# Performance work log

Measured on AMD Instinct MI355X. Metric: run time of the kernel, lower is better.

The kernel has to match this reference:

```python
import jax, jax.numpy as jnp
import numpy as np

B, T, DIM = 2, 2048, 2048
N_HEADS, N_KV_HEADS = 16, 4
HEAD_DIM = DIM // N_HEADS  # 128
N_REP = N_HEADS // N_KV_HEADS  # 4
ROPE_THETA = 10000.0


def setup_inputs() -> dict:
    key = jax.random.key(0)
    ks = jax.random.split(key, 5)
    x = jax.random.normal(ks[0], (B, T, DIM), dtype=jnp.float32)
    # RoPE tables (equivalent to complex freqs_cis = exp(i * t * inv_freq))
    inv_freq = 1.0 / (ROPE_THETA ** (np.arange(0, HEAD_DIM, 2, dtype=np.float32) / HEAD_DIM))
    t = np.arange(T, dtype=np.float32)
    ang = np.outer(t, inv_freq)  # (T, HEAD_DIM//2)
    freqs_cos = jnp.asarray(np.cos(ang), dtype=jnp.float32)
    freqs_sin = jnp.asarray(np.sin(ang), dtype=jnp.float32)
    s = 0.02
    wq = jax.random.normal(ks[1], (DIM, N_HEADS * HEAD_DIM), dtype=jnp.float32) * s
    wk = jax.random.normal(ks[2], (DIM, N_KV_HEADS * HEAD_DIM), dtype=jnp.float32) * s
    wv = jax.random.normal(ks[3], (DIM, N_KV_HEADS * HEAD_DIM), dtype=jnp.float32) * s
    wo = jax.random.normal(ks[4], (N_HEADS * HEAD_DIM, DIM), dtype=jnp.float32) * s
    return {"x": x, "freqs_cos": freqs_cos, "freqs_sin": freqs_sin,
            "wq": wq, "wk": wk, "wv": wv, "wo": wo}


def _apply_rope(t, cos, sin):
    # t: (B, H, T, hd); cos/sin: (T, hd//2); interleaved pairs like view_as_complex
    tr = t[..., 0::2]
    ti = t[..., 1::2]
    c = cos[None, None, :, :]
    s = sin[None, None, :, :]
    out_r = tr * c - ti * s
    out_i = tr * s + ti * c
    return jnp.stack([out_r, out_i], axis=-1).reshape(t.shape)


def reference(x, freqs_cos, freqs_sin, wq, wk, wv, wo):
    Bb, Tt, C = x.shape
    q = (x @ wq).reshape(Bb, Tt, N_HEADS, HEAD_DIM).transpose(0, 2, 1, 3)      # (B,H,T,hd)
    k = (x @ wk).reshape(Bb, Tt, N_KV_HEADS, HEAD_DIM).transpose(0, 2, 1, 3)   # (B,KV,T,hd)
    v = (x @ wv).reshape(Bb, Tt, N_KV_HEADS, HEAD_DIM).transpose(0, 2, 1, 3)
    q = _apply_rope(q, freqs_cos[:Tt], freqs_sin[:Tt])
    k = _apply_rope(k, freqs_cos[:Tt], freqs_sin[:Tt])
    # GQA repeat_kv
    k = jnp.repeat(k, N_REP, axis=1)  # (B,H,T,hd)
    v = jnp.repeat(v, N_REP, axis=1)
    scale = 1.0 / jnp.sqrt(jnp.float32(HEAD_DIM))
    scores = jnp.einsum("bhqd,bhkd->bhqk", q, k) * scale
    causal = jnp.tril(jnp.ones((Tt, Tt), dtype=bool))
    scores = jnp.where(causal[None, None], scores, jnp.float32(-jnp.inf))
    attn = jax.nn.softmax(scores, axis=-1)
    out = jnp.einsum("bhqk,bhkd->bhqd", attn, v)          # (B,H,T,hd)
    out = out.transpose(0, 2, 1, 3).reshape(Bb, Tt, C)
    return out @ wo
```

## Files before the change

kernel.cpp:

```cpp
#include <hip/hip_runtime.h>
#include <hip/hip_bf16.h>

#define SEQT 2048
#define NH 16
#define HD 128

typedef __bf16 bf16;
typedef __bf16 bf16x4 __attribute__((ext_vector_type(4)));
typedef __bf16 bf16x8 __attribute__((ext_vector_type(8)));
typedef float f32x4 __attribute__((ext_vector_type(4)));
typedef float f32x16 __attribute__((ext_vector_type(16)));

__device__ inline void glds16(const bf16* g, bf16* l) {
  __builtin_amdgcn_global_load_lds(
      (const __attribute__((address_space(1))) unsigned int*)g,
      (__attribute__((address_space(3))) unsigned int*)l, 16, 0, 0);
}

__device__ inline unsigned int cvtpk(float a, float b) {
  unsigned int d;
  asm("v_cvt_pk_bf16_f32 %0, %1, %2" : "=v"(d) : "v"(a), "v"(b));
  return d;
}

__global__ __launch_bounds__(256) void k_convert(const float* __restrict__ in,
                                                 bf16* __restrict__ out, int n8) {
  int i = blockIdx.x * 256 + threadIdx.x;
  if (i >= n8) return;
  const float4* p = (const float4*)in + (size_t)i * 2;
  float4 a = p[0], b = p[1];
  bf16x8 o;
  o[0] = (bf16)a.x; o[1] = (bf16)a.y; o[2] = (bf16)a.z; o[3] = (bf16)a.w;
  o[4] = (bf16)b.x; o[5] = (bf16)b.y; o[6] = (bf16)b.z; o[7] = (bf16)b.w;
  *((bf16x8*)out + i) = o;
}

__global__ __launch_bounds__(256) void k_transpose(const float* __restrict__ in,
                                                   bf16* __restrict__ out, int R, int C) {
  __shared__ float tile[32][33];
  int c0 = blockIdx.x * 32, r0 = blockIdx.y * 32;
  int tx = threadIdx.x, ty = threadIdx.y;
#pragma unroll
  for (int i = 0; i < 4; i++)
    tile[ty + i * 8][tx] = in[(size_t)(r0 + ty + i * 8) * C + c0 + tx];
  __syncthreads();
#pragma unroll
  for (int i = 0; i < 4; i++) {
    int r = ty + i * 8;
    out[(size_t)(c0 + r) * R + r0 + tx] = (bf16)tile[tx][r];
  }
}

__global__ __launch_bounds__(256) void k_transpose3(const float* __restrict__ wq,
                                                    const float* __restrict__ wk,
                                                    const float* __restrict__ wv,
                                                    bf16* __restrict__ W) {
  __shared__ float tile[32][33];
  int bx = blockIdx.x;
  const float* src;
  bf16* dst;
  int C;
  if (bx < 64) {
    src = wq; dst = W; C = 2048;
  } else if (bx < 80) {
    src = wk; dst = W + 2048 * 2048; C = 512; bx -= 64;
  } else {
    src = wv; dst = W + 2560 * 2048; C = 512; bx -= 80;
  }
  int c0 = bx * 32, r0 = blockIdx.y * 32;
  int tx = threadIdx.x, ty = threadIdx.y;
#pragma unroll
  for (int i = 0; i < 4; i++)
    tile[ty + i * 8][tx] = src[(size_t)(r0 + ty + i * 8) * C + c0 + tx];
  __syncthreads();
#pragma unroll
  for (int i = 0; i < 4; i++) {
    int r = ty + i * 8;
    dst[(size_t)(c0 + r) * 2048 + r0 + tx] = (bf16)tile[tx][r];
  }
}

template <typename OutT>
__global__ __launch_bounds__(256) void k_gemm(const bf16* __restrict__ A,
                                              const bf16* __restrict__ Bt,
                                              OutT* __restrict__ C,
                                              int M, int N, int K, int ldc) {
  __shared__ bf16 Al[128 * 32];
  __shared__ bf16 Bl[128 * 32];
  int tid = threadIdx.x;
  int m0 = blockIdx.y * 128, n0 = blockIdx.x * 128;
  int wid = tid >> 6, lane = tid & 63;
  int wr = (wid >> 1) * 64, wc = (wid & 1) * 64;
  int lr = lane & 15, lk = (lane >> 4) * 8;
  f32x4 acc[4][4] = {};

  for (int k0 = 0; k0 < K; k0 += 32) {
#pragma unroll
    for (int i = 0; i < 2; i++) {
      int idx = i * 256 + tid;
      int r = idx >> 2, kc = (idx & 3) * 8;
      glds16(A + (size_t)(m0 + r) * K + k0 + kc, Al + idx * 8);
      glds16(Bt + (size_t)(n0 + r) * K + k0 + kc, Bl + idx * 8);
    }
    __syncthreads();
    bf16x8 af[4], bfr[4];
#pragma unroll
    for (int mi = 0; mi < 4; mi++) af[mi] = *(const bf16x8*)&Al[(wr + mi * 16 + lr) * 32 + lk];
#pragma unroll
    for (int ni = 0; ni < 4; ni++) bfr[ni] = *(const bf16x8*)&Bl[(wc + ni * 16 + lr) * 32 + lk];
#pragma unroll
    for (int mi = 0; mi < 4; mi++)
#pragma unroll
      for (int ni = 0; ni < 4; ni++)
        acc[mi][ni] = __builtin_amdgcn_mfma_f32_16x16x32_bf16(af[mi], bfr[ni], acc[mi][ni], 0, 0, 0);
    __syncthreads();
  }

  int rbase = m0 + wr + ((lane >> 4) << 2);
#pragma unroll
  for (int mi = 0; mi < 4; mi++)
#pragma unroll
    for (int ni = 0; ni < 4; ni++)
#pragma unroll
      for (int r = 0; r < 4; r++) {
        int row = rbase + mi * 16 + r;
        int col = n0 + wc + ni * 16 + lr;
        C[(size_t)row * ldc + col] = (OutT)acc[mi][ni][r];
      }
}

__global__ __launch_bounds__(256) void k_rope(bf16* __restrict__ qkv,
                                              const float* __restrict__ fcos,
                                              const float* __restrict__ fsin) {
  int gid = blockIdx.x * 256 + threadIdx.x;
  int row = gid / 1280;
  int p = gid % 1280;
  int head = p >> 6;
  int dp = p & 63;
  int t = row & (SEQT - 1);
  int colbase = head < NH ? head * HD : NH * HD + (head - NH) * HD;
  bf16* ptr = qkv + (size_t)row * 3072 + colbase + dp * 2;
  float a = (float)ptr[0], b = (float)ptr[1];
  float c = fcos[t * 64 + dp], s = fsin[t * 64 + dp];
  ptr[0] = (bf16)(a * c - b * s);
  ptr[1] = (bf16)(a * s + b * c);
}

__global__ __launch_bounds__(256, 2) void k_attn(const bf16* __restrict__ qkv,
                                                 bf16* __restrict__ attout) {
  __shared__ bf16 Kl[2][8192];
  __shared__ bf16 Vt[128][72];
  __shared__ float Tabs[4][4][32];
  int bid = blockIdx.x;
  int qt = 31 - (bid >> 5);
  int bh = bid & 31;
  int b = bh >> 4, h = bh & 15, kvh = h >> 2;
  int tid = threadIdx.x, wid = tid >> 6, lane = tid & 63;
  int kvhalf = wid >> 1, wq = wid & 1;
  int li = lane & 31, hi = lane >> 5;
  int q0 = qt * 64;
  int qmin = q0 + wq * 32, qmax = qmin + 31;
  int qlane = qmin + li;
  const float C1 = 0.12751744979927212f;

  const bf16* kgbase = qkv + (size_t)b * SEQT * 3072 + 2048 + kvh * HD;
  const bf16* vgbase = kgbase + 512;

  bf16x8 qf[8];
  {
    const bf16* qb = qkv + (size_t)(b * SEQT + qlane) * 3072 + h * HD + hi * 8;
#pragma unroll
    for (int ks = 0; ks < 8; ks++) qf[ks] = *(const bf16x8*)(qb + ks * 16);
  }

  float mrun = -INFINITY, lpart = 0.f;
  f32x16 o0 = {}, o1 = {}, o2 = {}, o3 = {};
  int nkt = qt + 1;
  int kvbase = 32 * kvhalf;

  int g = (lane >> 4) & 3;
  int lr = lane & 15;
  int kq4 = (wid * 4 + g) * 4;
  int dc = lr * 8;
  int xr = (lr & 7) << 3;
  int kvw = kq4 ^ xr;

  bf16x8 vr0, vr1, vr2, vr3;

#pragma unroll
  for (int r = 0; r < 4; r++) {
    int ci = r * 256 + tid;
    int row = ci >> 4;
    int sl = (ci & 15) ^ (row & 15);
    glds16(kgbase + (size_t)row * 3072 + sl * 8, &Kl[0][ci * 8]);
  }
  {
    const bf16* vrow = vgbase + (size_t)kq4 * 3072 + dc;
    vr0 = *(const bf16x8*)(vrow);
    vr1 = *(const bf16x8*)(vrow + 3072);
    vr2 = *(const bf16x8*)(vrow + 6144);
    vr3 = *(const bf16x8*)(vrow + 9216);
  }

  for (int kt = 0; kt < nkt; kt++) {
    int cur = kt & 1;
    int kv0 = kt * 64;
    asm volatile("s_waitcnt vmcnt(0)" ::: "memory");

#pragma unroll
    for (int j = 0; j < 8; j++) {
      bf16x4 w;
      w[0] = vr0[j]; w[1] = vr1[j]; w[2] = vr2[j]; w[3] = vr3[j];
      *(bf16x4*)&Vt[dc + j][kvw] = w;
    }

    if (kt + 1 < nkt) {
      int kv1 = kv0 + 64;
      bf16* kdst = &Kl[cur ^ 1][0];
#pragma unroll
      for (int r = 0; r < 4; r++) {
        int ci = r * 256 + tid;
        int row = ci >> 4;
        int sl = (ci & 15) ^ (row & 15);
        glds16(kgbase + (size_t)(kv1 + row) * 3072 + sl * 8, kdst + ci * 8);
      }
      const bf16* vrow = vgbase + (size_t)(kv1 + kq4) * 3072 + dc;
      vr0 = *(const bf16x8*)(vrow);
      vr1 = *(const bf16x8*)(vrow + 3072);
      vr2 = *(const bf16x8*)(vrow + 6144);
      vr3 = *(const bf16x8*)(vrow + 9216);
    }

    asm volatile("s_waitcnt lgkmcnt(0)" ::: "memory");
    __builtin_amdgcn_sched_barrier(0);
    __builtin_amdgcn_s_barrier();
    __builtin_amdgcn_sched_barrier(0);

    if (kv0 + kvbase <= qmax) {
      f32x16 s0 = {};
      const char* kb0 = (const char*)&Kl[cur][0] + kvhalf * 8192 + li * 256;
      __builtin_amdgcn_s_setprio(1);
#pragma unroll
      for (int ks = 0; ks < 8; ks++) {
        int off = ((ks * 2 + hi) ^ (li & 15)) << 4;
        bf16x8 kf0 = *(const bf16x8*)(kb0 + off);
        s0 = __builtin_amdgcn_mfma_f32_32x32x16_bf16(kf0, qf[ks], s0, 0, 0, 0);
      }
      __builtin_amdgcn_s_setprio(0);

      if (kv0 + kvbase + 31 > qmin) {
        int base0 = kv0 + kvbase + 4 * hi - qlane;
#pragma unroll
        for (int r = 0; r < 16; r++) {
          int off = (r & 3) + 8 * (r >> 2);
          if (base0 + off > 0) s0[r] = -INFINITY;
        }
      }

      float pm = s0[0];
#pragma unroll
      for (int r = 1; r < 16; r++) pm = fmaxf(pm, s0[r]);
      pm = fmaxf(pm, __shfl_xor(pm, 32));

      if (!__all(pm - mrun <= 62.0f)) {
        float mnew = fmaxf(mrun, pm);
        float alpha = exp2f((mrun - mnew) * C1);
        mrun = mnew;
        lpart *= alpha;
        Tabs[0][wid][li] = alpha;
        asm volatile("s_waitcnt lgkmcnt(0)" ::: "memory");
        f32x4 a0 = *(const f32x4*)&Tabs[0][wid][4 * hi];
        f32x4 a1 = *(const f32x4*)&Tabs[0][wid][4 * hi + 8];
        f32x4 a2 = *(const f32x4*)&Tabs[0][wid][4 * hi + 16];
        f32x4 a3 = *(const f32x4*)&Tabs[0][wid][4 * hi + 24];
#define RESC_RR(rr, av)                                            \
  _Pragma("unroll") for (int i = 0; i < 4; i++) {                  \
    float f = av[i];                                               \
    o0[rr * 4 + i] *= f; o1[rr * 4 + i] *= f;                      \
    o2[rr * 4 + i] *= f; o3[rr * 4 + i] *= f;                      \
  }
        RESC_RR(0, a0) RESC_RR(1, a1) RESC_RR(2, a2) RESC_RR(3, a3)
#undef RESC_RR
      }

      float mC = mrun * C1;
      float rs = 0.f;
#pragma unroll
      for (int r = 0; r < 16; r++) {
        float p = exp2f(fmaf(s0[r], C1, -mC));
        s0[r] = p; rs += p;
      }
      lpart += rs;

      union U4 { unsigned int u[4]; bf16x8 v; };
      U4 pa0, pa1;
      {
        unsigned int e0 = cvtpk(s0[0], s0[1]), e1 = cvtpk(s0[2], s0[3]);
        unsigned int e2 = cvtpk(s0[4], s0[5]), e3 = cvtpk(s0[6], s0[7]);
        unsigned int e4 = cvtpk(s0[8], s0[9]), e5 = cvtpk(s0[10], s0[11]);
        unsigned int e6 = cvtpk(s0[12], s0[13]), e7 = cvtpk(s0[14], s0[15]);
        unsigned int t0 = __shfl_xor(e0, 32), t1 = __shfl_xor(e1, 32);
        unsigned int t2 = __shfl_xor(e2, 32), t3 = __shfl_xor(e3, 32);
        unsigned int t4 = __shfl_xor(e4, 32), t5 = __shfl_xor(e5, 32);
        unsigned int t6 = __shfl_xor(e6, 32), t7 = __shfl_xor(e7, 32);
        pa0.u[0] = hi ? t2 : e0;  pa0.u[1] = hi ? t3 : e1;
        pa0.u[2] = hi ? e2 : t0;  pa0.u[3] = hi ? e3 : t1;
        pa1.u[0] = hi ? t6 : e4;  pa1.u[1] = hi ? t7 : e5;
        pa1.u[2] = hi ? e6 : t4;  pa1.u[3] = hi ? e7 : t5;
      }

      __builtin_amdgcn_s_setprio(1);
#define PV_DB(OACC, DB)                                                      \
  {                                                                          \
    int d = DB * 32 + li;                                                    \
    int xv = ((d >> 3) & 7) << 3;                                            \
    bf16x8 vb0 = *(const bf16x8*)&Vt[d][(kvbase + hi * 8) ^ xv];             \
    bf16x8 vb1 = *(const bf16x8*)&Vt[d][(kvbase + 16 + hi * 8) ^ xv];        \
    OACC = __builtin_amdgcn_mfma_f32_32x32x16_bf16(pa0.v, vb0, OACC, 0, 0, 0); \
    OACC = __builtin_amdgcn_mfma_f32_32x32x16_bf16(pa1.v, vb1, OACC, 0, 0, 0); \
  }
      PV_DB(o0, 0) PV_DB(o1, 1) PV_DB(o2, 2) PV_DB(o3, 3)
#undef PV_DB
      __builtin_amdgcn_s_setprio(0);
    }

    __builtin_amdgcn_sched_barrier(0);
    __builtin_amdgcn_s_barrier();
    __builtin_amdgcn_sched_barrier(0);
  }

  lpart += __shfl_xor(lpart, 32);
  Tabs[0][wid][li] = mrun;
  Tabs[1][wid][li] = lpart;
  asm volatile("s_waitcnt lgkmcnt(0)" ::: "memory");
  __builtin_amdgcn_s_barrier();
  int peer = wid ^ 2;
  float mP = Tabs[0][peer][li], lP = Tabs[1][peer][li];
  float mS = fmaxf(mrun, mP);
  float fMe = exp2f((mrun - mS) * C1);
  float fPe = exp2f((mP - mS) * C1);
  float lTot = lpart * fMe + lP * fPe;
  Tabs[2][wid][li] = fMe;
  Tabs[3][wid][li] = 1.f / lTot;
  asm volatile("s_waitcnt lgkmcnt(0)" ::: "memory");
  __builtin_amdgcn_s_barrier();
  f32x4 Fv0 = *(const f32x4*)&Tabs[2][wid][4 * hi];
  f32x4 Fv1 = *(const f32x4*)&Tabs[2][wid][4 * hi + 8];
  f32x4 Fv2 = *(const f32x4*)&Tabs[2][wid][4 * hi + 16];
  f32x4 Fv3 = *(const f32x4*)&Tabs[2][wid][4 * hi + 24];
  f32x4 Iv0 = *(const f32x4*)&Tabs[3][wid][4 * hi];
  f32x4 Iv1 = *(const f32x4*)&Tabs[3][wid][4 * hi + 8];
  f32x4 Iv2 = *(const f32x4*)&Tabs[3][wid][4 * hi + 16];
  f32x4 Iv3 = *(const f32x4*)&Tabs[3][wid][4 * hi + 24];

  float* X = (float*)&Kl[0][0];
  float* Xb = X + (wid & 1) * 4096;
  if (kvhalf == 1) {
#define XW_RR(OACC, DB, rr, Fv)                                              \
  _Pragma("unroll") for (int i = 0; i < 4; i++)                              \
    Xb[(4 * hi + 8 * rr + i) * 128 + DB * 32 + li] = OACC[rr * 4 + i] * Fv[i];
#define XW_DB(OACC, DB) XW_RR(OACC, DB, 0, Fv0) XW_RR(OACC, DB, 1, Fv1) \
                        XW_RR(OACC, DB, 2, Fv2) XW_RR(OACC, DB, 3, Fv3)
    XW_DB(o0, 0) XW_DB(o1, 1) XW_DB(o2, 2) XW_DB(o3, 3)
#undef XW_DB
#undef XW_RR
  }
  asm volatile("s_waitcnt lgkmcnt(0)" ::: "memory");
  __builtin_amdgcn_s_barrier();
  if (kvhalf == 0) {
#define XR_RR(OACC, DB, rr, Fv)                                              \
  _Pragma("unroll") for (int i = 0; i < 4; i++)                              \
    OACC[rr * 4 + i] = OACC[rr * 4 + i] * Fv[i] +                            \
        Xb[(4 * hi + 8 * rr + i) * 128 + DB * 32 + li];
#define XR_DB(OACC, DB) XR_RR(OACC, DB, 0, Fv0) XR_RR(OACC, DB, 1, Fv1) \
                        XR_RR(OACC, DB, 2, Fv2) XR_RR(OACC, DB, 3, Fv3)
    XR_DB(o0, 0) XR_DB(o1, 1) XR_DB(o2, 2) XR_DB(o3, 3)
#undef XR_DB
#undef XR_RR
    size_t obase = (size_t)(b * SEQT) * 2048 + h * HD;
#define STORE_RR(rr, lv)                                                     \
  _Pragma("unroll") for (int i = 0; i < 4; i++) {                            \
    int q = qmin + 4 * hi + 8 * rr + i;                                      \
    size_t rowb = obase + (size_t)q * 2048 + li;                             \
    attout[rowb + 0]  = (bf16)(o0[rr * 4 + i] * lv[i]);                      \
    attout[rowb + 32] = (bf16)(o1[rr * 4 + i] * lv[i]);                      \
    attout[rowb + 64] = (bf16)(o2[rr * 4 + i] * lv[i]);                      \
    attout[rowb + 96] = (bf16)(o3[rr * 4 + i] * lv[i]);                      \
  }
    STORE_RR(0, Iv0) STORE_RR(1, Iv1) STORE_RR(2, Iv2) STORE_RR(3, Iv3)
#undef STORE_RR
  }
}

extern "C" void kernel_launch(void* const* d_in, const int* in_sizes, int n_in,
                              void* d_out, int out_size, void* d_ws, size_t ws_size,
                              hipStream_t stream) {
  const float* x    = (const float*)d_in[0];
  const float* fcos = (const float*)d_in[1];
  const float* fsin = (const float*)d_in[2];
  const float* wq   = (const float*)d_in[3];
  const float* wk   = (const float*)d_in[4];
  const float* wv   = (const float*)d_in[5];
  const float* wo   = (const float*)d_in[6];
  float* out = (float*)d_out;

  char* ws = (char*)d_ws;
  bf16* XB  = (bf16*)ws;
  bf16* W   = (bf16*)(ws + 16777216);
  bf16* QKV = (bf16*)(ws + 16777216 + 12582912);

  dim3 tb(32, 8);
  k_transpose3<<<dim3(96, 64), tb, 0, stream>>>(wq, wk, wv, W);
  k_convert<<<4096, 256, 0, stream>>>(x, XB, 1048576);
  k_gemm<bf16><<<dim3(24, 32), 256, 0, stream>>>(XB, W, QKV, 4096, 3072, 2048, 3072);
  k_rope<<<20480, 256, 0, stream>>>(QKV, fcos, fsin);
  k_attn<<<1024, 256, 0, stream>>>(QKV, XB);
  k_transpose<<<dim3(64, 64), tb, 0, stream>>>(wo, W, 2048, 2048);
  k_gemm<float><<<dim3(16, 32), 256, 0, stream>>>(XB, W, out, 4096, 2048, 2048, 2048);
}
```

Before: 227.0 us.

## Replace GEMM with 256x256 tiled, double-buffered 8-wave pipelined kernel

Replaces the simple 128x128 single-buffered GEMM with a 256x256-tile, 512-thread kernel. It double-buffers 64-wide K slices in LDS using an XOR swizzle, and interleaves async global-to-LDS loads with MFMA phases under explicit barriers and s_setprio. Block IDs are remapped for L2/XCD locality. The goal is to hide memory latency, cut LDS bank conflicts and raise data reuse in both projection GEMMs, at the cost of fewer blocks (192/128) and heavy LDS use (128KB).

After: 224.6 us. About the same (-1.0%).

```diff
diff --git a/kernel.cpp b/kernel.cpp
--- a/kernel.cpp
+++ b/kernel.cpp
@@ -81,52 +81,105 @@
 }
 
 template <typename OutT>
-__global__ __launch_bounds__(256) void k_gemm(const bf16* __restrict__ A,
-                                              const bf16* __restrict__ Bt,
-                                              OutT* __restrict__ C,
-                                              int M, int N, int K, int ldc) {
-  __shared__ bf16 Al[128 * 32];
-  __shared__ bf16 Bl[128 * 32];
+__global__ __launch_bounds__(512, 2) void k_gemm8(const bf16* __restrict__ A,
+                                                  const bf16* __restrict__ Bt,
+                                                  OutT* __restrict__ C,
+                                                  int nbx, int K, int ldc) {
+  __shared__ bf16 AB[2][2][16384];
+  int nb = gridDim.x;
+  int cpx = nb >> 3;
+  int bid = blockIdx.x;
+  int sw = (bid & 7) * cpx + (bid >> 3);
+  int bx = sw % nbx, by = sw / nbx;
+  int m0 = by << 8, n0 = bx << 8;
   int tid = threadIdx.x;
-  int m0 = blockIdx.y * 128, n0 = blockIdx.x * 128;
-  int wid = tid >> 6, lane = tid & 63;
-  int wr = (wid >> 1) * 64, wc = (wid & 1) * 64;
-  int lr = lane & 15, lk = (lane >> 4) * 8;
-  f32x4 acc[4][4] = {};
-
-  for (int k0 = 0; k0 < K; k0 += 32) {
-#pragma unroll
-    for (int i = 0; i < 2; i++) {
-      int idx = i * 256 + tid;
-      int r = idx >> 2, kc = (idx & 3) * 8;
-      glds16(A + (size_t)(m0 + r) * K + k0 + kc, Al + idx * 8);
-      glds16(Bt + (size_t)(n0 + r) * K + k0 + kc, Bl + idx * 8);
-    }
-    __syncthreads();
-    bf16x8 af[4], bfr[4];
-#pragma unroll
-    for (int mi = 0; mi < 4; mi++) af[mi] = *(const bf16x8*)&Al[(wr + mi * 16 + lr) * 32 + lk];
-#pragma unroll
-    for (int ni = 0; ni < 4; ni++) bfr[ni] = *(const bf16x8*)&Bl[(wc + ni * 16 + lr) * 32 + lk];
+  int lane = tid & 63, wid = tid >> 6;
+  int wr2 = wid >> 2, wc2 = wid & 3;
+  int lr = lane & 15, lg = lane >> 4;
+  int lx = lr & 7;
+
+  f32x4 acc[2][4][2][2] = {};
+
+  int srow = tid >> 3;
+  int ssl8 = ((tid & 7) ^ (srow & 7)) * 8;
+
+#define STAGE(SBUF, SAB, SHALF, KO)                                           \
+  {                                                                           \
+    int ko = (KO) <= (K - 64) ? (KO) : 0;                                     \
+    const bf16* gb = (SAB) ? Bt : A;                                          \
+    int rb = ((SAB) ? n0 : m0) + (SHALF) * 128 + srow;                        \
+    glds16(gb + (size_t)rb * K + ko + ssl8,                                   \
+           &AB[SBUF][SAB][(SHALF) * 8192 + tid * 8]);                         \
+    glds16(gb + (size_t)(rb + 64) * K + ko + ssl8,                            \
+           &AB[SBUF][SAB][(SHALF) * 8192 + (512 + tid) * 8]);                 \
+  }
+
+#define PHASE(BUF, QM, QN, SBUF, SAB, SHALF, SKO, DOVM)                       \
+  {                                                                           \
+    bf16x8 af[4][2], bq[2][2];                                                \
+    _Pragma("unroll") for (int mi = 0; mi < 4; mi++)                          \
+      _Pragma("unroll") for (int kk = 0; kk < 2; kk++)                        \
+        af[mi][kk] = *(const bf16x8*)&AB[BUF][0][                             \
+            ((QM) * 128 + wr2 * 64 + mi * 16 + lr) * 64 +                     \
+            (((kk * 4 + lg) ^ lx) * 8)];                                      \
+    _Pragma("unroll") for (int ni = 0; ni < 2; ni++)                          \
+      _Pragma("unroll") for (int kk = 0; kk < 2; kk++)                        \
+        bq[ni][kk] = *(const bf16x8*)&AB[BUF][1][                             \
+            ((QN) * 128 + wc2 * 32 + ni * 16 + lr) * 64 +                     \
+            (((kk * 4 + lg) ^ lx) * 8)];                                      \
+    STAGE(SBUF, SAB, SHALF, SKO)                                              \
+    if (DOVM) { asm volatile("s_waitcnt vmcnt(4)" ::: "memory"); }            \
+    __builtin_amdgcn_sched_barrier(0);                                        \
+    __builtin_amdgcn_s_barrier();                                             \
+    __builtin_amdgcn_sched_barrier(0);                                        \
+    __builtin_amdgcn_s_setprio(1);                                            \
+    _Pragma("unroll") for (int kk = 0; kk < 2; kk++)                          \
+      _Pragma("unroll") for (int mi = 0; mi < 4; mi++)                        \
+        _Pragma("unroll") for (int ni = 0; ni < 2; ni++)                      \
+          acc[QM][mi][QN][ni] = __builtin_amdgcn_mfma_f32_16x16x32_bf16(      \
+              af[mi][kk], bq[ni][kk], acc[QM][mi][QN][ni], 0, 0, 0);          \
+    __builtin_amdgcn_s_setprio(0);                                            \
+    __builtin_amdgcn_sched_barrier(0);                                        \
+    __builtin_amdgcn_s_barrier();                                             \
+    __builtin_amdgcn_sched_barrier(0);                                        \
+  }
+
+  STAGE(0, 0, 0, 0) STAGE(0, 1, 0, 0) STAGE(0, 0, 1, 0) STAGE(0, 1, 1, 0)
+  STAGE(1, 0, 0, 64) STAGE(1, 1, 0, 64)
+  asm volatile("s_waitcnt vmcnt(4)" ::: "memory");
+  __builtin_amdgcn_sched_barrier(0);
+  __builtin_amdgcn_s_barrier();
+  __builtin_amdgcn_sched_barrier(0);
+
+  int nit = K >> 7;
+  for (int it = 0; it < nit; it++) {
+    int kb = it << 7;
+    PHASE(0, 0, 0,  1, 0, 1, kb + 64,  0)
+    PHASE(0, 0, 1,  1, 1, 1, kb + 64,  0)
+    PHASE(0, 1, 0,  0, 0, 0, kb + 128, 0)
+    PHASE(0, 1, 1,  0, 1, 0, kb + 128, 1)
+    PHASE(1, 0, 0,  0, 0, 1, kb + 128, 0)
+    PHASE(1, 0, 1,  0, 1, 1, kb + 128, 0)
+    PHASE(1, 1, 0,  1, 0, 0, kb + 192, 0)
+    PHASE(1, 1, 1,  1, 1, 0, kb + 192, 1)
+  }
+#undef PHASE
+#undef STAGE
+
+  int crow = m0 + wr2 * 64 + lg * 4;
+  int ccol = n0 + wc2 * 32 + lr;
+#pragma unroll
+  for (int qm = 0; qm < 2; qm++)
 #pragma unroll
     for (int mi = 0; mi < 4; mi++)
 #pragma unroll
-      for (int ni = 0; ni < 4; ni++)
-        acc[mi][ni] = __builtin_amdgcn_mfma_f32_16x16x32_bf16(af[mi], bfr[ni], acc[mi][ni], 0, 0, 0);
-    __syncthreads();
-  }
-
-  int rbase = m0 + wr + ((lane >> 4) << 2);
-#pragma unroll
-  for (int mi = 0; mi < 4; mi++)
-#pragma unroll
-    for (int ni = 0; ni < 4; ni++)
-#pragma unroll
-      for (int r = 0; r < 4; r++) {
-        int row = rbase + mi * 16 + r;
-        int col = n0 + wc + ni * 16 + lr;
-        C[(size_t)row * ldc + col] = (OutT)acc[mi][ni][r];
-      }
+      for (int qn = 0; qn < 2; qn++)
+#pragma unroll
+        for (int ni = 0; ni < 2; ni++)
+#pragma unroll
+          for (int r = 0; r < 4; r++)
+            C[(size_t)(crow + qm * 128 + mi * 16 + r) * ldc +
+              ccol + qn * 128 + ni * 16] = (OutT)acc[qm][mi][qn][ni][r];
 }
 
 __global__ __launch_bounds__(256) void k_rope(bf16* __restrict__ qkv,
@@ -412,9 +465,9 @@
   dim3 tb(32, 8);
   k_transpose3<<<dim3(96, 64), tb, 0, stream>>>(wq, wk, wv, W);
   k_convert<<<4096, 256, 0, stream>>>(x, XB, 1048576);
-  k_gemm<bf16><<<dim3(24, 32), 256, 0, stream>>>(XB, W, QKV, 4096, 3072, 2048, 3072);
+  k_gemm8<bf16><<<192, 512, 0, stream>>>(XB, W, QKV, 12, 2048, 3072);
   k_rope<<<20480, 256, 0, stream>>>(QKV, fcos, fsin);
   k_attn<<<1024, 256, 0, stream>>>(QKV, XB);
   k_transpose<<<dim3(64, 64), tb, 0, stream>>>(wo, W, 2048, 2048);
-  k_gemm<float><<<dim3(16, 32), 256, 0, stream>>>(XB, W, out, 4096, 2048, 2048, 2048);
-}
+  k_gemm8<float><<<128, 512, 0, stream>>>(XB, W, out, 8, 2048, 2048);
+}
```
